# Optimization experiments

Hardware: AMD Instinct MI355X
Metric: run time of the kernel (lower is better)

The kernel has to match this reference:

```python
import jax, jax.numpy as jnp
import numpy as np

BATCH, SEQ_LEN, D_MODEL, STATE_DIM = 8, 4096, 512, 64
LN_EPS = 1e-5


def _hippo_log_neg_eigs(state_dim):
    A = np.zeros((state_dim, state_dim))
    for i in range(state_dim):
        for j in range(state_dim):
            if i > j:
                A[i, j] = -((2 * i + 1) ** 0.5) * ((2 * j + 1) ** 0.5)
            elif i == j:
                A[i, j] = -(i + 1)
    ev = np.sort(np.linalg.eigvals(A).real)[:state_dim]
    return np.log(-ev + 1e-06).astype(np.float32)


def setup_inputs() -> dict:
    key = jax.random.key(0)
    ks = jax.random.split(key, 8)
    d, s = D_MODEL, STATE_DIM
    return {
        "x": jax.random.normal(ks[0], (BATCH, SEQ_LEN, d), dtype=jnp.float32),
        "log_A": jnp.asarray(_hippo_log_neg_eigs(s)),
        "B": jax.random.normal(ks[1], (d, s), dtype=jnp.float32) * 0.01,
        "C": jax.random.normal(ks[2], (s, d), dtype=jnp.float32) * 0.01,
        "D": jnp.zeros((d,), dtype=jnp.float32),
        "log_dt": jnp.zeros((), dtype=jnp.float32),
        "gamma": jnp.ones((d,), dtype=jnp.float32),
        "beta": jnp.zeros((d,), dtype=jnp.float32),
        "W1": jax.random.normal(ks[3], (d, 2 * d), dtype=jnp.float32) * (1.0 / np.sqrt(d)),
        "b1": jnp.zeros((2 * d,), dtype=jnp.float32),
        "W2": jax.random.normal(ks[4], (2 * d, d), dtype=jnp.float32) * (1.0 / np.sqrt(2 * d)),
        "b2": jnp.zeros((d,), dtype=jnp.float32),
    }


def _layernorm(x, gamma, beta):
    mu = jnp.mean(x, axis=-1, keepdims=True)
    var = jnp.mean(jnp.square(x - mu), axis=-1, keepdims=True)
    return (x - mu) * jax.lax.rsqrt(var + LN_EPS) * gamma + beta


def reference(x, log_A, B, C, D, log_dt, gamma, beta, W1, b1, W2, b2):
    residual = x
    xn = _layernorm(x, gamma, beta)  # [B, L, D]

    dt = jnp.exp(log_dt)
    A_bar = jnp.exp(-jnp.exp(log_A) * dt)  # [S]

    # Precompute input projections for all timesteps, then scan the diagonal recurrence.
    xB = jnp.einsum("bld,ds->lbs", xn, B)  # [L, B, S]
    h0 = jnp.zeros((xn.shape[0], A_bar.shape[0]), dtype=xn.dtype)

    def step(h, xb_t):
        h = A_bar * h + xb_t
        return h, h

    _, hs = jax.lax.scan(step, h0, xB)  # hs: [L, B, S]

    y = jnp.einsum("lbs,sd->bld", hs, C) + xn * D  # [B, L, D]
    y = y + residual

    yn = _layernorm(y, gamma, beta)
    mlp = jax.nn.gelu(yn @ W1 + b1, approximate=False) @ W2 + b2
    return y + mlp
```

## Files before the change

kernel.cpp:

```cpp
#include <hip/hip_runtime.h>
#include <math.h>

#define BATCH 8
#define SEQL 4096
#define DMODEL 512
#define SDIM 64
#define MROWS (BATCH * SEQL)
#define LN_EPS 1e-5f

typedef __attribute__((ext_vector_type(8))) short bf16x8;
typedef __attribute__((ext_vector_type(4))) float f32x4;
typedef __attribute__((ext_vector_type(4))) int i32x4;

__device__ __forceinline__ float wave_sum(float v) {
#pragma unroll
  for (int off = 32; off > 0; off >>= 1) v += __shfl_xor(v, off, 64);
  return v;
}

__device__ __forceinline__ unsigned short f2bf(float f) {
  unsigned int u = __float_as_uint(f);
  u += 0x7fffu + ((u >> 16) & 1u);
  return (unsigned short)(u >> 16);
}

__device__ __forceinline__ float gelu_fast(float v) {
  float s = v * 0.70710678118654752f;
  float ax = fabsf(s);
  float t = 1.0f / (1.0f + 0.3275911f * ax);
  float p = ((((1.061405429f * t - 1.453152027f) * t + 1.421413741f) * t - 0.284496736f) * t +
             0.254829592f) *
            t;
  float er = 1.0f - p * __expf(-ax * ax);
  er = copysignf(er, s);
  return 0.5f * v * (1.0f + er);
}

__device__ __forceinline__ void gl2lds16(const void* g, void* l) {
  __builtin_amdgcn_global_load_lds((const __attribute__((address_space(1))) void*)g,
                                   (__attribute__((address_space(3))) void*)l, 16, 0, 0);
}

__device__ __forceinline__ unsigned lds_addr(const void* p) {
  return (unsigned)(uintptr_t)(__attribute__((address_space(3))) const void*)p;
}

__device__ __forceinline__ bf16x8 ldsr128(unsigned addr) {
  i32x4 r;
  asm volatile("ds_read_b128 %0, %1" : "=v"(r) : "v"(addr));
  union {
    i32x4 i;
    bf16x8 h;
  } u;
  u.i = r;
  return u.h;
}

__global__ void ln_stats_kernel(const float* __restrict__ x, float* __restrict__ mu,
                                float* __restrict__ rstd, unsigned short* __restrict__ xbf) {
  int row = blockIdx.x * 4 + (threadIdx.x >> 6);
  int lane = threadIdx.x & 63;
  const float4* xp = (const float4*)(x + (size_t)row * DMODEL);
  float4 a = xp[lane * 2];
  float4 b = xp[lane * 2 + 1];
  float s = a.x + a.y + a.z + a.w + b.x + b.y + b.z + b.w;
  float q = a.x * a.x + a.y * a.y + a.z * a.z + a.w * a.w + b.x * b.x + b.y * b.y +
            b.z * b.z + b.w * b.w;
  s = wave_sum(s);
  q = wave_sum(q);
  uint4 pk;
  pk.x = (unsigned)f2bf(a.x) | ((unsigned)f2bf(a.y) << 16);
  pk.y = (unsigned)f2bf(a.z) | ((unsigned)f2bf(a.w) << 16);
  pk.z = (unsigned)f2bf(b.x) | ((unsigned)f2bf(b.y) << 16);
  pk.w = (unsigned)f2bf(b.z) | ((unsigned)f2bf(b.w) << 16);
  ((uint4*)(xbf + (size_t)row * DMODEL))[lane] = pk;
  if (lane == 0) {
    float m = s * (1.0f / DMODEL);
    float var = q * (1.0f / DMODEL) - m * m;
    mu[row] = m;
    rstd[row] = rsqrtf(var + LN_EPS);
  }
}

__device__ __forceinline__ void transpose_body(const float* __restrict__ W,
                                               unsigned short* __restrict__ Wt, int K, int N,
                                               int bx, int by,
                                               unsigned short (*tile)[65]) {
  int k0 = by * 64, n0 = bx * 64;
  int tx = threadIdx.x & 15, ty = threadIdx.x >> 4;
#pragma unroll
  for (int p = 0; p < 4; ++p) {
    int k = p * 16 + ty;
    float4 v = *(const float4*)&W[(size_t)(k0 + k) * N + n0 + tx * 4];
    tile[tx * 4 + 0][k] = f2bf(v.x);
    tile[tx * 4 + 1][k] = f2bf(v.y);
    tile[tx * 4 + 2][k] = f2bf(v.z);
    tile[tx * 4 + 3][k] = f2bf(v.w);
  }
  __syncthreads();
#pragma unroll
  for (int p = 0; p < 4; ++p) {
    int n = p * 16 + ty;
    ushort4 o;
    o.x = tile[n][tx * 4 + 0];
    o.y = tile[n][tx * 4 + 1];
    o.z = tile[n][tx * 4 + 2];
    o.w = tile[n][tx * 4 + 3];
    *(ushort4*)&Wt[(size_t)(n0 + n) * K + k0 + tx * 4] = o;
  }
}

__global__ __launch_bounds__(256) void prep_all_kernel(
    const float* __restrict__ W1, const float* __restrict__ W2, const float* __restrict__ Cm,
    const float* __restrict__ Bm, const float* __restrict__ gamma,
    const float* __restrict__ beta, unsigned short* __restrict__ w1t,
    unsigned short* __restrict__ w2t, unsigned short* __restrict__ ctb,
    unsigned short* __restrict__ Bgt, float* __restrict__ gB, float* __restrict__ bB) {
  __shared__ unsigned short tile[64][65];
  int b = blockIdx.x;
  if (b < 128) {
    transpose_body(W1, w1t, 512, 1024, b & 15, b >> 4, tile);
  } else if (b < 256) {
    transpose_body(W2, w2t, 1024, 512, (b - 128) & 7, (b - 128) >> 3, tile);
  } else if (b < 264) {
    transpose_body(Cm, ctb, 64, 512, b - 256, 0, tile);
  } else {
    int s = (b - 264) * 4 + (threadIdx.x >> 6);
    int l = threadIdx.x & 63;
    float gs = 0.0f, bs = 0.0f;
    unsigned short tmp[8];
#pragma unroll
    for (int u = 0; u < 8; ++u) {
      int d = l * 8 + u;
      float bv = Bm[(size_t)d * SDIM + s];
      float gv = gamma[d], ev = beta[d];
      gs += gv * bv;
      bs += ev * bv;
      tmp[u] = f2bf(gv * bv);
    }
    *(ushort4*)&Bgt[(size_t)s * DMODEL + l * 8] = make_ushort4(tmp[0], tmp[1], tmp[2], tmp[3]);
    *(ushort4*)&Bgt[(size_t)s * DMODEL + l * 8 + 4] =
        make_ushort4(tmp[4], tmp[5], tmp[6], tmp[7]);
    gs = wave_sum(gs);
    bs = wave_sum(bs);
    if (l == 0) {
      gB[s] = gs;
      bB[s] = bs;
    }
  }
}

__global__ __launch_bounds__(256) void xb_mfma_kernel(
    const unsigned short* __restrict__ xbf, const unsigned short* __restrict__ Bgt,
    const float* __restrict__ mu, const float* __restrict__ rstd, const float* __restrict__ gB,
    const float* __restrict__ bB, float* __restrict__ xB) {
  __shared__ unsigned short As[128 * 32];
  __shared__ unsigned short Bs[64 * 32];
  const int t = threadIdx.x;
  const int wave = t >> 6, lane = t & 63;
  const int m0 = blockIdx.x * 128;
  const int wm = wave * 32;
  const int row = t >> 2, seg = t & 3;
  const int fr = lane & 15, fq = lane >> 4;
  f32x4 acc[2][4] = {};
  for (int k0 = 0; k0 < DMODEL; k0 += 32) {
    __syncthreads();
    gl2lds16(xbf + (size_t)(m0 + row) * DMODEL + k0 + seg * 8, As + (size_t)(wave * 16) * 32);
    gl2lds16(xbf + (size_t)(m0 + 64 + row) * DMODEL + k0 + seg * 8,
             As + (size_t)(64 + wave * 16) * 32);
    gl2lds16(Bgt + (size_t)row * DMODEL + k0 + seg * 8, Bs + (size_t)(wave * 16) * 32);
    __syncthreads();
#pragma unroll
    for (int i = 0; i < 2; ++i) {
      bf16x8 a = *(const bf16x8*)&As[(wm + i * 16 + fr) * 32 + fq * 8];
#pragma unroll
      for (int j = 0; j < 4; ++j) {
        bf16x8 b = *(const bf16x8*)&Bs[(j * 16 + fr) * 32 + fq * 8];
        acc[i][j] = __builtin_amdgcn_mfma_f32_16x16x32_bf16(a, b, acc[i][j], 0, 0, 0);
      }
    }
  }
#pragma unroll
  for (int i = 0; i < 2; ++i)
#pragma unroll
    for (int r = 0; r < 4; ++r) {
      const int m = m0 + wm + i * 16 + fq * 4 + r;
      const float rr = rstd[m], negmurr = -mu[m] * rstd[m];
#pragma unroll
      for (int j = 0; j < 4; ++j) {
        const int s = j * 16 + fr;
        xB[(size_t)m * SDIM + s] = rr * acc[i][j][r] + negmurr * gB[s] + bB[s];
      }
    }
}

__global__ void scan_ends_kernel(const float* __restrict__ xB, const float* __restrict__ logA,
                                 const float* __restrict__ logdt, float* __restrict__ ends) {
  int t = blockIdx.x * 128 + threadIdx.x;
  int s = t & 63;
  int c = (t >> 6) & 63;
  int b = t >> 12;
  float a = expf(-expf(logA[s]) * expf(logdt[0]));
  const float* p = xB + ((size_t)(b * SEQL + c * 64)) * SDIM + s;
  float e = 0.0f;
#pragma unroll
  for (int i = 0; i < 64; ++i) e = a * e + p[(size_t)i * SDIM];
  ends[(b * 64 + c) * 64 + s] = e;
}

__global__ void scan_fix_kernel(const float* __restrict__ logA, const float* __restrict__ logdt,
                                const float* __restrict__ ends, const float* __restrict__ xB,
                                unsigned short* __restrict__ hsb) {
  int t = blockIdx.x * 128 + threadIdx.x;
  int s = t & 63;
  int c = (t >> 6) & 63;
  int b = t >> 12;
  float a = expf(-expf(logA[s]) * expf(logdt[0]));
  float a64 = a;
#pragma unroll
  for (int i = 0; i < 6; ++i) a64 *= a64;
  float h = 0.0f;
  for (int cp = 0; cp < c; ++cp) h = a64 * h + ends[(b * 64 + cp) * 64 + s];
  const float* p = xB + ((size_t)(b * SEQL + c * 64)) * SDIM + s;
  unsigned short* q = hsb + ((size_t)(b * SEQL + c * 64)) * SDIM + s;
#pragma unroll
  for (int i = 0; i < 64; ++i) {
    h = a * h + p[(size_t)i * SDIM];
    q[(size_t)i * SDIM] = f2bf(h);
  }
}

__global__ __launch_bounds__(512, 2) void y_ln_fused_kernel(
    const unsigned short* __restrict__ hsb, const unsigned short* __restrict__ ctb,
    const float* __restrict__ x, const float* __restrict__ mu1,
    const float* __restrict__ rstd1, const float* __restrict__ gamma,
    const float* __restrict__ beta, const float* __restrict__ Dv, float* __restrict__ out,
    unsigned short* __restrict__ yn) {
  __shared__ alignas(16) unsigned short As[128 * 64];
  __shared__ alignas(16) unsigned short Bs[512 * 64];
  __shared__ float rsum[128], rsq[128];
  const int t = threadIdx.x;
  const int wid = t >> 6, lane = t & 63;
  const int m0 = blockIdx.x * 128;
  const int wm = (wid >> 2) * 64;
  const int wn = (wid & 3) * 128;
  const int fr = lane & 15, fq = lane >> 4;
  const int srow = t >> 3;
  const int ksw = ((t & 7) ^ ((t >> 3) & 7)) << 3;
  gl2lds16(hsb + (size_t)(m0 + srow) * 64 + ksw, &As[(wid * 8) * 64]);
  gl2lds16(hsb + (size_t)(m0 + 64 + srow) * 64 + ksw, &As[(64 + wid * 8) * 64]);
#pragma unroll
  for (int h = 0; h < 8; ++h)
    gl2lds16(ctb + (size_t)(h * 64 + srow) * 64 + ksw, &Bs[(h * 64 + wid * 8) * 64]);
  if (t < 128) {
    rsum[t] = 0.0f;
    rsq[t] = 0.0f;
  }
  asm volatile("s_waitcnt vmcnt(0)" ::: "memory");
  __builtin_amdgcn_s_barrier();

  f32x4 acc[4][8] = {};
#pragma unroll
  for (int s = 0; s < 2; ++s) {
    bf16x8 af[4], bf[8];
#pragma unroll
    for (int i = 0; i < 4; ++i)
      af[i] = *(const bf16x8*)&As[(wm + i * 16 + fr) * 64 + ((s * 4 + fq) ^ (fr & 7)) * 8];
#pragma unroll
    for (int j = 0; j < 8; ++j)
      bf[j] = *(const bf16x8*)&Bs[(wn + j * 16 + fr) * 64 + ((s * 4 + fq) ^ (fr & 7)) * 8];
#pragma unroll
    for (int i = 0; i < 4; ++i)
#pragma unroll
      for (int j = 0; j < 8; ++j)
        acc[i][j] = __builtin_amdgcn_mfma_f32_16x16x32_bf16(af[i], bf[j], acc[i][j], 0, 0, 0);
  }

  float ga[8], be[8], dd[8];
#pragma unroll
  for (int j = 0; j < 8; ++j) {
    const int cg = wn + j * 16 + fr;
    ga[j] = gamma[cg];
    be[j] = beta[cg];
    dd[j] = Dv[cg];
  }
  float ps[4][4], pq[4][4];
#pragma unroll
  for (int i = 0; i < 4; ++i)
#pragma unroll
    for (int r = 0; r < 4; ++r) {
      const int m = m0 + wm + i * 16 + fq * 4 + r;
      const float mu = mu1[m], rs = rstd1[m];
      float s1 = 0.0f, s2 = 0.0f;
#pragma unroll
      for (int j = 0; j < 8; ++j) {
        const int cg = wn + j * 16 + fr;
        const float xv = x[(size_t)m * DMODEL + cg];
        float yv = acc[i][j][r] + ((xv - mu) * rs * ga[j] + be[j]) * dd[j] + xv;
        out[(size_t)m * DMODEL + cg] = yv;
        acc[i][j][r] = yv;
        s1 += yv;
        s2 += yv * yv;
      }
      ps[i][r] = s1;
      pq[i][r] = s2;
    }
#pragma unroll
  for (int i = 0; i < 4; ++i)
#pragma unroll
    for (int r = 0; r < 4; ++r) {
#pragma unroll
      for (int off = 1; off < 16; off <<= 1) {
        ps[i][r] += __shfl_xor(ps[i][r], off, 64);
        pq[i][r] += __shfl_xor(pq[i][r], off, 64);
      }
    }
  if (fr == 0) {
#pragma unroll
    for (int i = 0; i < 4; ++i)
#pragma unroll
      for (int r = 0; r < 4; ++r) {
        atomicAdd(&rsum[wm + i * 16 + fq * 4 + r], ps[i][r]);
        atomicAdd(&rsq[wm + i * 16 + fq * 4 + r], pq[i][r]);
      }
  }
  __syncthreads();
#pragma unroll
  for (int i = 0; i < 4; ++i)
#pragma unroll
    for (int r = 0; r < 4; ++r) {
      const int rl = wm + i * 16 + fq * 4 + r;
      const int m = m0 + rl;
      const float mu2 = rsum[rl] * (1.0f / DMODEL);
      const float var = rsq[rl] * (1.0f / DMODEL) - mu2 * mu2;
      const float rs2 = rsqrtf(var + LN_EPS);
#pragma unroll
      for (int j = 0; j < 8; ++j) {
        const int cg = wn + j * 16 + fr;
        yn[(size_t)m * DMODEL + cg] = f2bf((acc[i][j][r] - mu2) * rs2 * ga[j] + be[j]);
      }
    }
}

template <int K, int NALL, int EPI>
__global__ __launch_bounds__(512, 2) void gemm256_kernel(
    const unsigned short* __restrict__ Am, const unsigned short* __restrict__ Bm,
    const float* __restrict__ bias, unsigned short* __restrict__ gout,
    float* __restrict__ out) {
  __shared__ alignas(16) unsigned short As[2][256 * 64];
  __shared__ alignas(16) unsigned short Bs[2][256 * 64];
  const int t = threadIdx.x;
  const int wid = t >> 6, lane = t & 63;
  const int nwg = gridDim.x * gridDim.y;
  const int orig = blockIdx.y * gridDim.x + blockIdx.x;
  const int swz = (orig & 7) * (nwg >> 3) + (orig >> 3);
  const int m0 = (swz / gridDim.x) * 256, n0 = (swz % gridDim.x) * 256;
  const int wm = (wid >> 2) * 128, wn = (wid & 3) * 64;
  const int fr = lane & 15, fq = lane >> 4;
  constexpr int NT = K / 64;
  const int srow = t >> 3;
  const int ksw = ((t & 7) ^ ((t >> 3) & 7)) << 3;

  auto stageA = [&](int bb, int h, int kt) {
    const unsigned short* s0 = Am + (size_t)(m0 + h * 128 + srow) * K + kt * 64 + ksw;
    gl2lds16(s0, &As[bb][(h * 128 + wid * 8) * 64]);
    gl2lds16(s0 + (size_t)64 * K, &As[bb][(h * 128 + 64 + wid * 8) * 64]);
  };
  auto stageB = [&](int bb, int h, int kt) {
    const unsigned short* s0 = Bm + (size_t)(n0 + h * 128 + srow) * K + kt * 64 + ksw;
    gl2lds16(s0, &Bs[bb][(h * 128 + wid * 8) * 64]);
    gl2lds16(s0 + (size_t)64 * K, &Bs[bb][(h * 128 + 64 + wid * 8) * 64]);
  };

  const unsigned aA0 = lds_addr(&As[0][0]) + (unsigned)((wm + fr) * 128 + (fq ^ (fr & 7)) * 16);
  const unsigned aA1 =
      lds_addr(&As[0][0]) + (unsigned)((wm + fr) * 128 + ((4 + fq) ^ (fr & 7)) * 16);
  const unsigned aB0 = lds_addr(&Bs[0][0]) + (unsigned)((wn + fr) * 128 + (fq ^ (fr & 7)) * 16);
  const unsigned aB1 =
      lds_addr(&Bs[0][0]) + (unsigned)((wn + fr) * 128 + ((4 + fq) ^ (fr & 7)) * 16);

  stageA(0, 0, 0);
  stageA(0, 1, 0);
  stageB(0, 0, 0);
  stageB(0, 1, 0);
  asm volatile("s_waitcnt vmcnt(0)" ::: "memory");
  __builtin_amdgcn_s_barrier();

  bf16x8 a0[8], b0[4], a1[8], b1[4];
#pragma unroll
  for (int i = 0; i < 8; ++i) a0[i] = ldsr128(aA0 + i * 2048);
#pragma unroll
  for (int j = 0; j < 4; ++j) b0[j] = ldsr128(aB0 + j * 2048);

  f32x4 acc[8][4] = {};
  for (int c = 0; c < NT; ++c) {
    const unsigned bo = (unsigned)((c & 1) << 15);
    const unsigned bn = bo ^ 32768u;
#pragma unroll
    for (int i = 0; i < 8; ++i) a1[i] = ldsr128(aA1 + bo + i * 2048);
#pragma unroll
    for (int j = 0; j < 4; ++j) b1[j] = ldsr128(aB1 + bo + j * 2048);
    if (c + 1 < NT) {
      const int nb = (c & 1) ^ 1;
      stageA(nb, 0, c + 1);
      stageA(nb, 1, c + 1);
      stageB(nb, 0, c + 1);
      stageB(nb, 1, c + 1);
    }
    asm volatile("s_waitcnt lgkmcnt(12)" ::: "memory");
    __builtin_amdgcn_sched_barrier(0);
    __builtin_amdgcn_s_setprio(1);
#pragma unroll
    for (int i = 0; i < 8; ++i)
#pragma unroll
      for (int j = 0; j < 4; ++j)
        acc[i][j] = __builtin_amdgcn_mfma_f32_16x16x32_bf16(a0[i], b0[j], acc[i][j], 0, 0, 0);
    __builtin_amdgcn_s_setprio(0);
    __builtin_amdgcn_sched_barrier(0);
    if (c + 1 < NT) {
      asm volatile("s_waitcnt vmcnt(0)" ::: "memory");
      __builtin_amdgcn_s_barrier();
#pragma unroll
      for (int i = 0; i < 8; ++i) a0[i] = ldsr128(aA0 + bn + i * 2048);
#pragma unroll
      for (int j = 0; j < 4; ++j) b0[j] = ldsr128(aB0 + bn + j * 2048);
      asm volatile("s_waitcnt lgkmcnt(12)" ::: "memory");
    } else {
      asm volatile("s_waitcnt lgkmcnt(0)" ::: "memory");
    }
    __builtin_amdgcn_sched_barrier(0);
    __builtin_amdgcn_s_setprio(1);
#pragma unroll
    for (int i = 0; i < 8; ++i)
#pragma unroll
      for (int j = 0; j < 4; ++j)
        acc[i][j] = __builtin_amdgcn_mfma_f32_16x16x32_bf16(a1[i], b1[j], acc[i][j], 0, 0, 0);
    __builtin_amdgcn_s_setprio(0);
    if (c + 1 < NT) __builtin_amdgcn_s_barrier();
  }

#pragma unroll
  for (int i = 0; i < 8; ++i)
#pragma unroll
    for (int j = 0; j < 4; ++j) {
      const int cg = n0 + wn + j * 16 + fr;
      const float bb = bias[cg];
#pragma unroll
      for (int r = 0; r < 4; ++r) {
        const int rg = m0 + wm + i * 16 + fq * 4 + r;
        if (EPI == 0) {
          gout[(size_t)rg * NALL + cg] = f2bf(gelu_fast(acc[i][j][r] + bb));
        } else {
          const size_t off = (size_t)rg * NALL + cg;
          out[off] = out[off] + acc[i][j][r] + bb;
        }
      }
    }
}

extern "C" void kernel_launch(void* const* d_in, const int* in_sizes, int n_in, void* d_out,
                              int out_size, void* d_ws, size_t ws_size, hipStream_t stream) {
  const float* x = (const float*)d_in[0];
  const float* logA = (const float*)d_in[1];
  const float* Bm = (const float*)d_in[2];
  const float* Cm = (const float*)d_in[3];
  const float* Dv = (const float*)d_in[4];
  const float* logdt = (const float*)d_in[5];
  const float* gamma = (const float*)d_in[6];
  const float* beta = (const float*)d_in[7];
  const float* W1 = (const float*)d_in[8];
  const float* b1 = (const float*)d_in[9];
  const float* W2 = (const float*)d_in[10];
  const float* b2 = (const float*)d_in[11];
  float* out = (float*)d_out;

  char* ws = (char*)d_ws;
  float* mu1 = (float*)(ws + 0);
  float* rstd1 = (float*)(ws + 131072);
  float* ends = (float*)(ws + 262144);
  float* gB = (float*)(ws + 524288);
  float* bB = (float*)(ws + 524800);
  unsigned short* Bgt = (unsigned short*)(ws + 525312);
  unsigned short* ctb = (unsigned short*)(ws + 590848);
  unsigned short* w1t = (unsigned short*)(ws + 656384);
  unsigned short* w2t = (unsigned short*)(ws + 1704960);
  unsigned short* g = (unsigned short*)(ws + 2753536);
  unsigned short* xbf = (unsigned short*)(ws + 2753536);
  float* xB = (float*)(ws + 69862400);
  unsigned short* hsb = (unsigned short*)(ws + 78251008);
  unsigned short* yn = (unsigned short*)(ws + 82445312);

  prep_all_kernel<<<280, 256, 0, stream>>>(W1, W2, Cm, Bm, gamma, beta, w1t, w2t, ctb, Bgt, gB,
                                           bB);
  ln_stats_kernel<<<MROWS / 4, 256, 0, stream>>>(x, mu1, rstd1, xbf);
  xb_mfma_kernel<<<MROWS / 128, 256, 0, stream>>>(xbf, Bgt, mu1, rstd1, gB, bB, xB);
  scan_ends_kernel<<<256, 128, 0, stream>>>(xB, logA, logdt, ends);
  scan_fix_kernel<<<256, 128, 0, stream>>>(logA, logdt, ends, xB, hsb);
  y_ln_fused_kernel<<<MROWS / 128, 512, 0, stream>>>(hsb, ctb, x, mu1, rstd1, gamma, beta, Dv,
                                                     out, yn);
  gemm256_kernel<512, 1024, 0><<<dim3(1024 / 256, MROWS / 256), 512, 0, stream>>>(
      yn, w1t, b1, g, nullptr);
  gemm256_kernel<1024, 512, 1><<<dim3(512 / 256, MROWS / 256), 512, 0, stream>>>(
      g, w2t, b2, nullptr, out);
}
```

Measured before the change: 321.2 us.

## Replace 256x256 pipelined GEMM with simpler 128x128 tile GEMM

Both MLP GEMMs change from a 256x256-tile, 512-thread kernel to a 128x128-tile, 256-thread kernel. The hand-scheduled register double-buffering of LDS fragments is replaced by plain compiler-generated LDS reads inside each k-step. This gives more, smaller workgroups and a simpler schedule. The cost is lower data reuse per tile and less overlap between LDS reads and MFMA.

```diff
diff --git a/kernel.cpp b/kernel.cpp
--- a/kernel.cpp
+++ b/kernel.cpp
@@ -10,7 +10,6 @@
 
 typedef __attribute__((ext_vector_type(8))) short bf16x8;
 typedef __attribute__((ext_vector_type(4))) float f32x4;
-typedef __attribute__((ext_vector_type(4))) int i32x4;
 
 __device__ __forceinline__ float wave_sum(float v) {
 #pragma unroll
@@ -39,21 +38,6 @@
 __device__ __forceinline__ void gl2lds16(const void* g, void* l) {
   __builtin_amdgcn_global_load_lds((const __attribute__((address_space(1))) void*)g,
                                    (__attribute__((address_space(3))) void*)l, 16, 0, 0);
-}
-
-__device__ __forceinline__ unsigned lds_addr(const void* p) {
-  return (unsigned)(uintptr_t)(__attribute__((address_space(3))) const void*)p;
-}
-
-__device__ __forceinline__ bf16x8 ldsr128(unsigned addr) {
-  i32x4 r;
-  asm volatile("ds_read_b128 %0, %1" : "=v"(r) : "v"(addr));
-  union {
-    i32x4 i;
-    bf16x8 h;
-  } u;
-  u.i = r;
-  return u.h;
 }
 
 __global__ void ln_stats_kernel(const float* __restrict__ x, float* __restrict__ mu,
@@ -343,104 +327,81 @@
 }
 
 template <int K, int NALL, int EPI>
-__global__ __launch_bounds__(512, 2) void gemm256_kernel(
+__global__ __launch_bounds__(256, 2) void gemm128_kernel(
     const unsigned short* __restrict__ Am, const unsigned short* __restrict__ Bm,
     const float* __restrict__ bias, unsigned short* __restrict__ gout,
     float* __restrict__ out) {
-  __shared__ alignas(16) unsigned short As[2][256 * 64];
-  __shared__ alignas(16) unsigned short Bs[2][256 * 64];
+  __shared__ alignas(16) unsigned short As[2][128 * 64];
+  __shared__ alignas(16) unsigned short Bs[2][128 * 64];
   const int t = threadIdx.x;
   const int wid = t >> 6, lane = t & 63;
   const int nwg = gridDim.x * gridDim.y;
   const int orig = blockIdx.y * gridDim.x + blockIdx.x;
   const int swz = (orig & 7) * (nwg >> 3) + (orig >> 3);
-  const int m0 = (swz / gridDim.x) * 256, n0 = (swz % gridDim.x) * 256;
-  const int wm = (wid >> 2) * 128, wn = (wid & 3) * 64;
+  const int m0 = (swz / gridDim.x) * 128, n0 = (swz % gridDim.x) * 128;
+  const int wm = (wid >> 1) * 64, wn = (wid & 1) * 64;
   const int fr = lane & 15, fq = lane >> 4;
   constexpr int NT = K / 64;
   const int srow = t >> 3;
   const int ksw = ((t & 7) ^ ((t >> 3) & 7)) << 3;
 
-  auto stageA = [&](int bb, int h, int kt) {
-    const unsigned short* s0 = Am + (size_t)(m0 + h * 128 + srow) * K + kt * 64 + ksw;
-    gl2lds16(s0, &As[bb][(h * 128 + wid * 8) * 64]);
-    gl2lds16(s0 + (size_t)64 * K, &As[bb][(h * 128 + 64 + wid * 8) * 64]);
+  auto stageA = [&](int bb, int kt) {
+    const unsigned short* s0 = Am + (size_t)(m0 + srow) * K + kt * 64 + ksw;
+#pragma unroll
+    for (int q = 0; q < 4; ++q)
+      gl2lds16(s0 + (size_t)(q * 32) * K, &As[bb][(q * 32 + wid * 8) * 64]);
   };
-  auto stageB = [&](int bb, int h, int kt) {
-    const unsigned short* s0 = Bm + (size_t)(n0 + h * 128 + srow) * K + kt * 64 + ksw;
-    gl2lds16(s0, &Bs[bb][(h * 128 + wid * 8) * 64]);
-    gl2lds16(s0 + (size_t)64 * K, &Bs[bb][(h * 128 + 64 + wid * 8) * 64]);
+  auto stageB = [&](int bb, int kt) {
+    const unsigned short* s0 = Bm + (size_t)(n0 + srow) * K + kt * 64 + ksw;
+#pragma unroll
+    for (int q = 0; q < 4; ++q)
+      gl2lds16(s0 + (size_t)(q * 32) * K, &Bs[bb][(q * 32 + wid * 8) * 64]);
   };
 
-  const unsigned aA0 = lds_addr(&As[0][0]) + (unsigned)((wm + fr) * 128 + (fq ^ (fr & 7)) * 16);
-  const unsigned aA1 =
-      lds_addr(&As[0][0]) + (unsigned)((wm + fr) * 128 + ((4 + fq) ^ (fr & 7)) * 16);
-  const unsigned aB0 = lds_addr(&Bs[0][0]) + (unsigned)((wn + fr) * 128 + (fq ^ (fr & 7)) * 16);
-  const unsigned aB1 =
-      lds_addr(&Bs[0][0]) + (unsigned)((wn + fr) * 128 + ((4 + fq) ^ (fr & 7)) * 16);
-
-  stageA(0, 0, 0);
-  stageA(0, 1, 0);
-  stageB(0, 0, 0);
-  stageB(0, 1, 0);
+  stageA(0, 0);
+  stageB(0, 0);
   asm volatile("s_waitcnt vmcnt(0)" ::: "memory");
   __builtin_amdgcn_s_barrier();
-
-  bf16x8 a0[8], b0[4], a1[8], b1[4];
-#pragma unroll
-  for (int i = 0; i < 8; ++i) a0[i] = ldsr128(aA0 + i * 2048);
-#pragma unroll
-  for (int j = 0; j < 4; ++j) b0[j] = ldsr128(aB0 + j * 2048);
-
-  f32x4 acc[8][4] = {};
+  __builtin_amdgcn_sched_barrier(0);
+
+  f32x4 acc[4][4] = {};
   for (int c = 0; c < NT; ++c) {
-    const unsigned bo = (unsigned)((c & 1) << 15);
-    const unsigned bn = bo ^ 32768u;
-#pragma unroll
-    for (int i = 0; i < 8; ++i) a1[i] = ldsr128(aA1 + bo + i * 2048);
-#pragma unroll
-    for (int j = 0; j < 4; ++j) b1[j] = ldsr128(aB1 + bo + j * 2048);
+    const int b = c & 1;
     if (c + 1 < NT) {
-      const int nb = (c & 1) ^ 1;
-      stageA(nb, 0, c + 1);
-      stageA(nb, 1, c + 1);
-      stageB(nb, 0, c + 1);
-      stageB(nb, 1, c + 1);
-    }
-    asm volatile("s_waitcnt lgkmcnt(12)" ::: "memory");
-    __builtin_amdgcn_sched_barrier(0);
+      stageA(b ^ 1, c + 1);
+      stageB(b ^ 1, c + 1);
+    }
+    bf16x8 av[2][4], bv[2][4];
+#pragma unroll
+    for (int s = 0; s < 2; ++s) {
+#pragma unroll
+      for (int i = 0; i < 4; ++i)
+        av[s][i] =
+            *(const bf16x8*)&As[b][(wm + i * 16 + fr) * 64 + ((s * 4 + fq) ^ (fr & 7)) * 8];
+#pragma unroll
+      for (int j = 0; j < 4; ++j)
+        bv[s][j] =
+            *(const bf16x8*)&Bs[b][(wn + j * 16 + fr) * 64 + ((s * 4 + fq) ^ (fr & 7)) * 8];
+    }
     __builtin_amdgcn_s_setprio(1);
 #pragma unroll
-    for (int i = 0; i < 8; ++i)
-#pragma unroll
-      for (int j = 0; j < 4; ++j)
-        acc[i][j] = __builtin_amdgcn_mfma_f32_16x16x32_bf16(a0[i], b0[j], acc[i][j], 0, 0, 0);
+    for (int s = 0; s < 2; ++s)
+#pragma unroll
+      for (int i = 0; i < 4; ++i)
+#pragma unroll
+        for (int j = 0; j < 4; ++j)
+          acc[i][j] =
+              __builtin_amdgcn_mfma_f32_16x16x32_bf16(av[s][i], bv[s][j], acc[i][j], 0, 0, 0);
     __builtin_amdgcn_s_setprio(0);
-    __builtin_amdgcn_sched_barrier(0);
     if (c + 1 < NT) {
       asm volatile("s_waitcnt vmcnt(0)" ::: "memory");
       __builtin_amdgcn_s_barrier();
-#pragma unroll
-      for (int i = 0; i < 8; ++i) a0[i] = ldsr128(aA0 + bn + i * 2048);
-#pragma unroll
-      for (int j = 0; j < 4; ++j) b0[j] = ldsr128(aB0 + bn + j * 2048);
-      asm volatile("s_waitcnt lgkmcnt(12)" ::: "memory");
-    } else {
-      asm volatile("s_waitcnt lgkmcnt(0)" ::: "memory");
-    }
-    __builtin_amdgcn_sched_barrier(0);
-    __builtin_amdgcn_s_setprio(1);
-#pragma unroll
-    for (int i = 0; i < 8; ++i)
-#pragma unroll
-      for (int j = 0; j < 4; ++j)
-        acc[i][j] = __builtin_amdgcn_mfma_f32_16x16x32_bf16(a1[i], b1[j], acc[i][j], 0, 0, 0);
-    __builtin_amdgcn_s_setprio(0);
-    if (c + 1 < NT) __builtin_amdgcn_s_barrier();
-  }
-
-#pragma unroll
-  for (int i = 0; i < 8; ++i)
+      __builtin_amdgcn_sched_barrier(0);
+    }
+  }
+
+#pragma unroll
+  for (int i = 0; i < 4; ++i)
 #pragma unroll
     for (int j = 0; j < 4; ++j) {
       const int cg = n0 + wn + j * 16 + fr;
@@ -498,8 +459,8 @@
   scan_fix_kernel<<<256, 128, 0, stream>>>(logA, logdt, ends, xB, hsb);
   y_ln_fused_kernel<<<MROWS / 128, 512, 0, stream>>>(hsb, ctb, x, mu1, rstd1, gamma, beta, Dv,
                                                      out, yn);
-  gemm256_kernel<512, 1024, 0><<<dim3(1024 / 256, MROWS / 256), 512, 0, stream>>>(
+  gemm128_kernel<512, 1024, 0><<<dim3(1024 / 128, MROWS / 128), 256, 0, stream>>>(
       yn, w1t, b1, g, nullptr);
-  gemm256_kernel<1024, 512, 1><<<dim3(512 / 256, MROWS / 256), 512, 0, stream>>>(
+  gemm128_kernel<1024, 512, 1><<<dim3(512 / 128, MROWS / 128), 256, 0, stream>>>(
       g, w2t, b2, nullptr, out);
 }
```

Measured after the change: 317.1 us. About the same (-1.3%).
